# Optimization experiments

Hardware: AMD Instinct MI355X
Metric: run time of the kernel (lower is better)

## Reference

```python
import jax, jax.numpy as jnp
import numpy as np

B, T, D, H = 8, 2048, 1024, 128


def setup_inputs() -> dict:
    key = jax.random.key(0)
    k1, k2, k3, k4 = jax.random.split(key, 4)
    x = jax.random.normal(k1, (B, T, D), dtype=jnp.float32)
    # nn.Linear(D, H, bias=False): y = x @ W.T with W [H, D]; we store W as [D, H]
    Wq = jax.random.normal(k2, (D, H), dtype=jnp.float32) * (1.0 / np.sqrt(D))
    Wk = jax.random.normal(k3, (D, H), dtype=jnp.float32) * (1.0 / np.sqrt(D))
    Wv = jax.random.normal(k4, (D, H), dtype=jnp.float32) * (1.0 / np.sqrt(D))
    return {"x": x, "Wq": Wq, "Wk": Wk, "Wv": Wv}


def reference(x, Wq, Wk, Wv):
    # q, k, v projections (bias-free)
    q = jnp.einsum("btd,dh->bth", x, Wq)
    k = jnp.einsum("btd,dh->bth", x, Wk)
    v = jnp.einsum("btd,dh->bth", x, Wv)
    scale = 1.0 / jnp.sqrt(jnp.asarray(q.shape[-1], dtype=q.dtype))
    # full T x T score matrix, as in the original module
    scores = jnp.einsum("bqh,bkh->bqk", q, k) * scale
    T_ = x.shape[1]
    causal = jnp.tril(jnp.ones((T_, T_), dtype=bool))
    scores = jnp.where(causal[None, :, :], scores, -jnp.inf)
    weights = jax.nn.softmax(scores, axis=-1)
    # dropout is identity in eval mode (deterministic reference)
    return jnp.einsum("bqk,bkh->bqh", weights, v)
```

## Files before the change

kernel.cpp:

```cpp
#include <hip/hip_runtime.h>

typedef float  f32x4  __attribute__((ext_vector_type(4)));
typedef __bf16 bf16x8 __attribute__((ext_vector_type(8)));
typedef unsigned short u16;
typedef unsigned int   u32;
typedef u32 u32x4 __attribute__((ext_vector_type(4)));
typedef u16 u16x4 __attribute__((ext_vector_type(4)));
typedef u16 u16x8 __attribute__((ext_vector_type(8)));
typedef float f32x4v __attribute__((ext_vector_type(4)));

#define B_ 8
#define T_ 2048
#define D_ 1024
#define H_ 128
#define M_ (B_ * T_)

__device__ __forceinline__ u16 f2b(float f) {
  u32 u = __builtin_bit_cast(u32, f);
  u32 r = u + 0x7fffu + ((u >> 16) & 1u);
  return (u16)(r >> 16);
}

__device__ __forceinline__ void gl2lds16(const void* g, void* l) {
  __builtin_amdgcn_global_load_lds(
      (const __attribute__((address_space(1))) void*)g,
      (__attribute__((address_space(3))) void*)l, 16, 0, 0);
}

__global__ __launch_bounds__(256) void wt_kernel(const float* __restrict__ Wq,
                                                 const float* __restrict__ Wk,
                                                 const float* __restrict__ Wv,
                                                 u16* __restrict__ ws) {
  __shared__ u16 Ld[128 * 136];
  const float* W = (blockIdx.y == 0) ? Wq : (blockIdx.y == 1) ? Wk : Wv;
  u16* Wt = ws + (size_t)blockIdx.y * (D_ * H_);
  const int d0 = blockIdx.x * 128;
  const int t = threadIdx.x;
  for (int i = 0; i < 16; ++i) {
    int idx = i * 256 + t;
    int d = idx >> 5, h4 = (idx & 31) * 4;
    f32x4v wv = *(const f32x4v*)(W + (size_t)(d0 + d) * H_ + h4);
    u16x4 bv;
    bv[0] = f2b(wv[0]); bv[1] = f2b(wv[1]); bv[2] = f2b(wv[2]); bv[3] = f2b(wv[3]);
    *(u16x4*)(&Ld[d * 136 + h4]) = bv;
  }
  __syncthreads();
  for (int i = 0; i < 8; ++i) {
    int idx = i * 256 + t;
    int h = idx >> 4, d8 = (idx & 15) * 8;
    u16x8 ov;
    for (int j = 0; j < 8; ++j) ov[j] = Ld[(d8 + j) * 136 + h];
    *(u16x8*)(Wt + (size_t)h * D_ + d0 + d8) = ov;
  }
}

__global__ __launch_bounds__(512, 4) void qkv_gemm(const float* __restrict__ x,
                                                   const u16* __restrict__ Wt_all,
                                                   u16* __restrict__ Qb,
                                                   u16* __restrict__ Kb,
                                                   u16* __restrict__ Vt) {
  __shared__ __attribute__((aligned(16))) u16 As[2][64 * 40];
  __shared__ __attribute__((aligned(16))) u16 Bs[2][192 * 40];
  const int m0 = (int)(blockIdx.x >> 1) * 64;
  const int n0 = (int)(blockIdx.x & 1) * 192;
  const int t = threadIdx.x;
  const int lane = t & 63;
  const int w = t >> 6;
  const int wm = (w & 1) * 32, wn = (w >> 1) * 48;
  const int li = lane & 15, q4 = lane >> 4;

  const int arow = t >> 3, ac4 = (t & 7) * 4;

  f32x4 acc[2][3];
  for (int i = 0; i < 2; ++i)
    for (int j = 0; j < 3; ++j) acc[i][j] = (f32x4){0.f, 0.f, 0.f, 0.f};

  f32x4v areg[2];
  u16x4 breg[2][3];

  auto load_tiles = [&](int kt, int s) {
    const int k0 = kt * 32;
    areg[s] = *(const f32x4v*)(x + (size_t)(m0 + arow) * D_ + k0 + ac4);
    for (int i2 = 0; i2 < 3; ++i2) {
      int idx = i2 * 512 + t;
      int row = idx >> 3, c4 = (idx & 7) * 4;
      breg[s][i2] = *(const u16x4*)(Wt_all + (size_t)(n0 + row) * D_ + k0 + c4);
    }
  };

  load_tiles(0, 0);
  load_tiles(1, 1);
  for (int kt = 0; kt < 32; ++kt) {
    const int s = kt & 1;
    {
      u16x4 av;
      av[0] = f2b(areg[s][0]); av[1] = f2b(areg[s][1]);
      av[2] = f2b(areg[s][2]); av[3] = f2b(areg[s][3]);
      *(u16x4*)(&As[s][arow * 40 + ac4]) = av;
    }
    for (int i2 = 0; i2 < 3; ++i2) {
      int idx = i2 * 512 + t;
      int row = idx >> 3, c4 = (idx & 7) * 4;
      *(u16x4*)(&Bs[s][row * 40 + c4]) = breg[s][i2];
    }
    __syncthreads();
    if (kt + 2 < 32) load_tiles(kt + 2, s);

    bf16x8 af[2];
    for (int i = 0; i < 2; ++i)
      af[i] = *(const bf16x8*)(&As[s][(wm + i * 16 + li) * 40 + q4 * 8]);
    for (int j = 0; j < 3; ++j) {
      bf16x8 bfr = *(const bf16x8*)(&Bs[s][(wn + j * 16 + li) * 40 + q4 * 8]);
      for (int i = 0; i < 2; ++i)
        acc[i][j] = __builtin_amdgcn_mfma_f32_16x16x32_bf16(af[i], bfr, acc[i][j], 0, 0, 0);
    }
  }

  const float qs = 0.12751740696864213f;
  const int bb = m0 >> 11;
  const int tl0 = (m0 & (T_ - 1)) + wm + q4 * 4;
  for (int j = 0; j < 3; ++j) {
    int n = n0 + wn + j * 16 + li;
    int p = n >> 7, col = n & 127;
    if (p == 2) {
      for (int i = 0; i < 2; ++i) {
        u16x4 pv;
        for (int r = 0; r < 4; ++r) pv[r] = f2b(acc[i][j][r]);
        *(u16x4*)(Vt + (size_t)bb * (H_ * T_) + (size_t)col * T_ + tl0 + i * 16) = pv;
      }
    } else {
      u16* dst = (p == 0) ? Qb : Kb;
      float s = (p == 0) ? qs : 1.0f;
      for (int i = 0; i < 2; ++i)
        for (int r = 0; r < 4; ++r) {
          int mg = m0 + wm + i * 16 + q4 * 4 + r;
          dst[(size_t)mg * H_ + col] = f2b(acc[i][j][r] * s);
        }
    }
  }
}

#define NSLOT_PER_B 36

__device__ __forceinline__ int slot_base(int qt) {
  return (qt < 8) ? 2 * (qt - 4) : (qt < 12) ? 8 + 3 * (qt - 8) : 20 + 4 * (qt - 12);
}

__global__ __launch_bounds__(512, 2) void flash_split(const u16* __restrict__ Qb,
                                                      const u16* __restrict__ Kb,
                                                      const u16* __restrict__ Vt,
                                                      float* __restrict__ Opart,
                                                      float* __restrict__ Ls,
                                                      float* __restrict__ out) {
  __shared__ __attribute__((aligned(16))) u16 Ks[64 * 128];
  __shared__ __attribute__((aligned(16))) u16 Vs[128 * 64];
  __shared__ __attribute__((aligned(16))) u16 Ps[128 * 72];

  int xb = blockIdx.x, qt = 15, split = 0;
  for (int q = 15; q >= 0; --q) {
    int ns = (2 * q + 9) >> 3;
    if (xb < ns) { qt = q; split = xb; break; }
    xb -= ns;
  }
  const int b = blockIdx.y;
  const int nkv = 2 * qt + 2;
  const int nsplit = (2 * qt + 9) >> 3;
  const int kv0t = split * 8;
  const int kv1t = (kv0t + 8 < nkv) ? kv0t + 8 : nkv;
  const int q0 = qt * 128;

  const int t = threadIdx.x;
  const int lane = t & 63;
  const int w = t >> 6;
  const int li = lane & 15, q4 = lane >> 4;

  bf16x8 qf[4];
  const int qrow = b * T_ + q0 + w * 16 + li;
  for (int kk = 0; kk < 4; ++kk)
    qf[kk] = *(const bf16x8*)(Qb + (size_t)qrow * H_ + kk * 32 + q4 * 8);

  f32x4 oacc[8];
  for (int i = 0; i < 8; ++i) oacc[i] = (f32x4){0.f, 0.f, 0.f, 0.f};
  float rs[4] = {0.f, 0.f, 0.f, 0.f};

  for (int jt = kv0t; jt < kv1t; ++jt) {
    const int j0 = jt * 64;
    __syncthreads();
    for (int i = 0; i < 2; ++i) {
      int seg = i * 8 + w;
      {
        int r = seg * 4 + (lane >> 4);
        int c = (lane & 15) ^ (r & 7);
        gl2lds16(Kb + (size_t)(b * T_ + j0 + r) * H_ + c * 8, &Ks[seg << 9]);
      }
      {
        int r = seg * 8 + (lane >> 3);
        int c = (lane & 7) ^ (r & 7);
        gl2lds16(Vt + (size_t)b * (H_ * T_) + (size_t)r * T_ + j0 + c * 8,
                 &Vs[seg << 9]);
      }
    }
    __syncthreads();

    f32x4 sacc[4];
    for (int jn = 0; jn < 4; ++jn) sacc[jn] = (f32x4){0.f, 0.f, 0.f, 0.f};
    for (int jn = 0; jn < 4; ++jn) {
      int row = jn * 16 + li;
      for (int kk = 0; kk < 4; ++kk) {
        int phys = ((kk << 2) | q4) ^ (row & 7);
        bf16x8 kf = *(const bf16x8*)(&Ks[row * 128 + phys * 8]);
        sacc[jn] = __builtin_amdgcn_mfma_f32_16x16x32_bf16(qf[kk], kf, sacc[jn], 0, 0, 0);
      }
    }

    if (jt >= 2 * qt) {
      for (int jn = 0; jn < 4; ++jn) {
        int jg = j0 + jn * 16 + li;
        for (int r = 0; r < 4; ++r) {
          int qg = q0 + w * 16 + q4 * 4 + r;
          if (jg > qg) sacc[jn][r] = -1e30f;
        }
      }
    }

    for (int jn = 0; jn < 4; ++jn)
      for (int r = 0; r < 4; ++r) {
        float p = exp2f(sacc[jn][r]);
        rs[r] += p;
        Ps[(w * 16 + q4 * 4 + r) * 72 + jn * 16 + li] = f2b(p);
      }

    for (int ks = 0; ks < 2; ++ks) {
      bf16x8 pa = *(const bf16x8*)(&Ps[(w * 16 + li) * 72 + ks * 32 + q4 * 8]);
      for (int hn = 0; hn < 8; ++hn) {
        int row = hn * 16 + li;
        int phys = ((ks << 2) | q4) ^ (row & 7);
        bf16x8 vf = *(const bf16x8*)(&Vs[row * 64 + phys * 8]);
        oacc[hn] = __builtin_amdgcn_mfma_f32_16x16x32_bf16(pa, vf, oacc[hn], 0, 0, 0);
      }
    }
  }

  float lr[4];
  for (int r = 0; r < 4; ++r) {
    float s = rs[r];
    for (int off = 1; off < 16; off <<= 1) s += __shfl_xor(s, off, 16);
    lr[r] = s;
  }

  if (nsplit == 1) {
    for (int hn = 0; hn < 8; ++hn)
      for (int r = 0; r < 4; ++r) {
        int qg = b * T_ + q0 + w * 16 + q4 * 4 + r;
        out[(size_t)qg * H_ + hn * 16 + li] = oacc[hn][r] / lr[r];
      }
  } else {
    const int slot = b * NSLOT_PER_B + slot_base(qt) + split;
    float* Od = Opart + (size_t)slot * (128 * 128);
    for (int hn = 0; hn < 8; ++hn)
      for (int r = 0; r < 4; ++r) {
        int qq = w * 16 + q4 * 4 + r;
        Od[qq * 128 + hn * 16 + li] = oacc[hn][r];
      }
    if (li == 0)
      for (int r = 0; r < 4; ++r)
        Ls[slot * 128 + w * 16 + q4 * 4 + r] = lr[r];
  }
}

__global__ __launch_bounds__(512) void flash_merge(const float* __restrict__ Opart,
                                                   const float* __restrict__ Ls,
                                                   float* __restrict__ out) {
  __shared__ float inv_l[128];
  const int qt = 4 + blockIdx.x;
  const int b = blockIdx.y;
  const int nsplit = (2 * qt + 9) >> 3;
  const int slot0 = b * NSLOT_PER_B + slot_base(qt);
  const int t = threadIdx.x;

  if (t < 128) {
    float L = 0.f;
    for (int s = 0; s < nsplit; ++s) L += Ls[(slot0 + s) * 128 + t];
    inv_l[t] = 1.0f / L;
  }
  __syncthreads();

  float* dst = out + ((size_t)b * T_ + (size_t)qt * 128) * H_;
  for (int i = 0; i < 8; ++i) {
    int e4 = i * 512 + t;
    int q = e4 >> 5;
    f32x4 acc = (f32x4){0.f, 0.f, 0.f, 0.f};
    for (int s = 0; s < nsplit; ++s) {
      f32x4 v = *(const f32x4*)(Opart + (size_t)(slot0 + s) * (128 * 128) + e4 * 4);
      acc[0] += v[0]; acc[1] += v[1]; acc[2] += v[2]; acc[3] += v[3];
    }
    float inv = inv_l[q];
    acc[0] *= inv; acc[1] *= inv; acc[2] *= inv; acc[3] *= inv;
    *(f32x4*)(dst + e4 * 4) = acc;
  }
}

extern "C" void kernel_launch(void* const* d_in, const int* in_sizes, int n_in,
                              void* d_out, int out_size, void* d_ws, size_t ws_size,
                              hipStream_t stream) {
  const float* x  = (const float*)d_in[0];
  const float* Wq = (const float*)d_in[1];
  const float* Wk = (const float*)d_in[2];
  const float* Wv = (const float*)d_in[3];
  float* out = (float*)d_out;

  u16* ws = (u16*)d_ws;
  u16* WtAll = ws;
  u16* Qb = ws + 3 * (size_t)(D_ * H_);
  u16* Kb = Qb + (size_t)M_ * H_;
  u16* Vt = Kb + (size_t)M_ * H_;
  float* Opart = (float*)(Vt + (size_t)M_ * H_);
  float* Ls = Opart + (size_t)8 * NSLOT_PER_B * 128 * 128;

  wt_kernel<<<dim3(8, 3), 256, 0, stream>>>(Wq, Wk, Wv, WtAll);
  qkv_gemm<<<dim3(512), 512, 0, stream>>>(x, WtAll, Qb, Kb, Vt);
  flash_split<<<dim3(40, 8), 512, 0, stream>>>(Qb, Kb, Vt, Opart, Ls, out);
  flash_merge<<<dim3(12, 8), 512, 0, stream>>>(Opart, Ls, out);
}
```

Baseline: 173.8 us.

## Double-buffer K/V in flash kernel, stage GEMM B tiles directly to LDS

The flash attention kernel now double-buffers the K and V tiles in shared memory. The next tile's direct global-to-LDS loads are issued right after the barrier, so they overlap the current tile's MFMA work. The QKV GEMM loads the weight tile straight into a swizzled, unpadded LDS layout, which removes the register round trip. It also cuts the A prefetch to one tile ahead. The weight transpose kernel uses smaller 32-row blocks to launch more workgroups. Doubling K/V LDS raises shared memory use per block and may lower occupancy. The shallower A prefetch can expose global load latency in the GEMM.

```diff
diff --git a/kernel.cpp b/kernel.cpp
--- a/kernel.cpp
+++ b/kernel.cpp
@@ -31,12 +31,12 @@
                                                  const float* __restrict__ Wk,
                                                  const float* __restrict__ Wv,
                                                  u16* __restrict__ ws) {
-  __shared__ u16 Ld[128 * 136];
+  __shared__ u16 Ld[32 * 136];
   const float* W = (blockIdx.y == 0) ? Wq : (blockIdx.y == 1) ? Wk : Wv;
   u16* Wt = ws + (size_t)blockIdx.y * (D_ * H_);
-  const int d0 = blockIdx.x * 128;
+  const int d0 = blockIdx.x * 32;
   const int t = threadIdx.x;
-  for (int i = 0; i < 16; ++i) {
+  for (int i = 0; i < 4; ++i) {
     int idx = i * 256 + t;
     int d = idx >> 5, h4 = (idx & 31) * 4;
     f32x4v wv = *(const f32x4v*)(W + (size_t)(d0 + d) * H_ + h4);
@@ -45,9 +45,9 @@
     *(u16x4*)(&Ld[d * 136 + h4]) = bv;
   }
   __syncthreads();
-  for (int i = 0; i < 8; ++i) {
+  for (int i = 0; i < 2; ++i) {
     int idx = i * 256 + t;
-    int h = idx >> 4, d8 = (idx & 15) * 8;
+    int h = idx >> 2, d8 = (idx & 3) * 8;
     u16x8 ov;
     for (int j = 0; j < 8; ++j) ov[j] = Ld[(d8 + j) * 136 + h];
     *(u16x8*)(Wt + (size_t)h * D_ + d0 + d8) = ov;
@@ -60,7 +60,7 @@
                                                    u16* __restrict__ Kb,
                                                    u16* __restrict__ Vt) {
   __shared__ __attribute__((aligned(16))) u16 As[2][64 * 40];
-  __shared__ __attribute__((aligned(16))) u16 Bs[2][192 * 40];
+  __shared__ __attribute__((aligned(16))) u16 Bs[2][192 * 32];
   const int m0 = (int)(blockIdx.x >> 1) * 64;
   const int n0 = (int)(blockIdx.x & 1) * 192;
   const int t = threadIdx.x;
@@ -68,49 +68,46 @@
   const int w = t >> 6;
   const int wm = (w & 1) * 32, wn = (w >> 1) * 48;
   const int li = lane & 15, q4 = lane >> 4;
-
   const int arow = t >> 3, ac4 = (t & 7) * 4;
+  const int br = lane >> 2, bu = lane & 3;
+  const int bul = bu ^ ((br >> 1) & 3);
 
   f32x4 acc[2][3];
   for (int i = 0; i < 2; ++i)
     for (int j = 0; j < 3; ++j) acc[i][j] = (f32x4){0.f, 0.f, 0.f, 0.f};
 
-  f32x4v areg[2];
-  u16x4 breg[2][3];
-
-  auto load_tiles = [&](int kt, int s) {
-    const int k0 = kt * 32;
-    areg[s] = *(const f32x4v*)(x + (size_t)(m0 + arow) * D_ + k0 + ac4);
-    for (int i2 = 0; i2 < 3; ++i2) {
-      int idx = i2 * 512 + t;
-      int row = idx >> 3, c4 = (idx & 7) * 4;
-      breg[s][i2] = *(const u16x4*)(Wt_all + (size_t)(n0 + row) * D_ + k0 + c4);
-    }
+  f32x4v areg;
+  auto load_a = [&](int kt) {
+    areg = *(const f32x4v*)(x + (size_t)(m0 + arow) * D_ + kt * 32 + ac4);
   };
-
-  load_tiles(0, 0);
-  load_tiles(1, 1);
+  auto stage_b = [&](int kt, int sb) {
+    for (int ii = 0; ii < 2; ++ii) {
+      int seg = ii * 8 + w;
+      if (seg < 12)
+        gl2lds16(Wt_all + (size_t)(n0 + seg * 16 + br) * D_ + kt * 32 + bul * 8,
+                 &Bs[sb][seg * 512]);
+    }
+  };
+
+  load_a(0);
+  stage_b(0, 0);
   for (int kt = 0; kt < 32; ++kt) {
     const int s = kt & 1;
     {
       u16x4 av;
-      av[0] = f2b(areg[s][0]); av[1] = f2b(areg[s][1]);
-      av[2] = f2b(areg[s][2]); av[3] = f2b(areg[s][3]);
+      av[0] = f2b(areg[0]); av[1] = f2b(areg[1]);
+      av[2] = f2b(areg[2]); av[3] = f2b(areg[3]);
       *(u16x4*)(&As[s][arow * 40 + ac4]) = av;
     }
-    for (int i2 = 0; i2 < 3; ++i2) {
-      int idx = i2 * 512 + t;
-      int row = idx >> 3, c4 = (idx & 7) * 4;
-      *(u16x4*)(&Bs[s][row * 40 + c4]) = breg[s][i2];
-    }
     __syncthreads();
-    if (kt + 2 < 32) load_tiles(kt + 2, s);
+    if (kt + 1 < 32) { load_a(kt + 1); stage_b(kt + 1, s ^ 1); }
 
     bf16x8 af[2];
     for (int i = 0; i < 2; ++i)
       af[i] = *(const bf16x8*)(&As[s][(wm + i * 16 + li) * 40 + q4 * 8]);
     for (int j = 0; j < 3; ++j) {
-      bf16x8 bfr = *(const bf16x8*)(&Bs[s][(wn + j * 16 + li) * 40 + q4 * 8]);
+      int R = wn + j * 16 + li;
+      bf16x8 bfr = *(const bf16x8*)(&Bs[s][R * 32 + (q4 ^ ((li >> 1) & 3)) * 8]);
       for (int i = 0; i < 2; ++i)
         acc[i][j] = __builtin_amdgcn_mfma_f32_16x16x32_bf16(af[i], bfr, acc[i][j], 0, 0, 0);
     }
@@ -130,11 +127,11 @@
       }
     } else {
       u16* dst = (p == 0) ? Qb : Kb;
-      float s = (p == 0) ? qs : 1.0f;
+      float sc = (p == 0) ? qs : 1.0f;
       for (int i = 0; i < 2; ++i)
         for (int r = 0; r < 4; ++r) {
           int mg = m0 + wm + i * 16 + q4 * 4 + r;
-          dst[(size_t)mg * H_ + col] = f2b(acc[i][j][r] * s);
+          dst[(size_t)mg * H_ + col] = f2b(acc[i][j][r] * sc);
         }
     }
   }
@@ -152,8 +149,8 @@
                                                       float* __restrict__ Opart,
                                                       float* __restrict__ Ls,
                                                       float* __restrict__ out) {
-  __shared__ __attribute__((aligned(16))) u16 Ks[64 * 128];
-  __shared__ __attribute__((aligned(16))) u16 Vs[128 * 64];
+  __shared__ __attribute__((aligned(16))) u16 Ks[2][64 * 128];
+  __shared__ __attribute__((aligned(16))) u16 Vs[2][128 * 64];
   __shared__ __attribute__((aligned(16))) u16 Ps[128 * 72];
 
   int xb = blockIdx.x, qt = 15, split = 0;
@@ -183,24 +180,30 @@
   for (int i = 0; i < 8; ++i) oacc[i] = (f32x4){0.f, 0.f, 0.f, 0.f};
   float rs[4] = {0.f, 0.f, 0.f, 0.f};
 
-  for (int jt = kv0t; jt < kv1t; ++jt) {
+  auto stage = [&](int jt, int sb) {
     const int j0 = jt * 64;
-    __syncthreads();
     for (int i = 0; i < 2; ++i) {
       int seg = i * 8 + w;
       {
         int r = seg * 4 + (lane >> 4);
         int c = (lane & 15) ^ (r & 7);
-        gl2lds16(Kb + (size_t)(b * T_ + j0 + r) * H_ + c * 8, &Ks[seg << 9]);
+        gl2lds16(Kb + (size_t)(b * T_ + j0 + r) * H_ + c * 8, &Ks[sb][seg << 9]);
       }
       {
         int r = seg * 8 + (lane >> 3);
         int c = (lane & 7) ^ (r & 7);
         gl2lds16(Vt + (size_t)b * (H_ * T_) + (size_t)r * T_ + j0 + c * 8,
-                 &Vs[seg << 9]);
-      }
-    }
+                 &Vs[sb][seg << 9]);
+      }
+    }
+  };
+
+  stage(kv0t, 0);
+  for (int jt = kv0t; jt < kv1t; ++jt) {
+    const int buf = (jt - kv0t) & 1;
+    const int j0 = jt * 64;
     __syncthreads();
+    if (jt + 1 < kv1t) stage(jt + 1, buf ^ 1);
 
     f32x4 sacc[4];
     for (int jn = 0; jn < 4; ++jn) sacc[jn] = (f32x4){0.f, 0.f, 0.f, 0.f};
@@ -208,7 +211,7 @@
       int row = jn * 16 + li;
       for (int kk = 0; kk < 4; ++kk) {
         int phys = ((kk << 2) | q4) ^ (row & 7);
-        bf16x8 kf = *(const bf16x8*)(&Ks[row * 128 + phys * 8]);
+        bf16x8 kf = *(const bf16x8*)(&Ks[buf][row * 128 + phys * 8]);
         sacc[jn] = __builtin_amdgcn_mfma_f32_16x16x32_bf16(qf[kk], kf, sacc[jn], 0, 0, 0);
       }
     }
@@ -235,7 +238,7 @@
       for (int hn = 0; hn < 8; ++hn) {
         int row = hn * 16 + li;
         int phys = ((ks << 2) | q4) ^ (row & 7);
-        bf16x8 vf = *(const bf16x8*)(&Vs[row * 64 + phys * 8]);
+        bf16x8 vf = *(const bf16x8*)(&Vs[buf][row * 64 + phys * 8]);
         oacc[hn] = __builtin_amdgcn_mfma_f32_16x16x32_bf16(pa, vf, oacc[hn], 0, 0, 0);
       }
     }
@@ -317,7 +320,7 @@
   float* Opart = (float*)(Vt + (size_t)M_ * H_);
   float* Ls = Opart + (size_t)8 * NSLOT_PER_B * 128 * 128;
 
-  wt_kernel<<<dim3(8, 3), 256, 0, stream>>>(Wq, Wk, Wv, WtAll);
+  wt_kernel<<<dim3(32, 3), 256, 0, stream>>>(Wq, Wk, Wv, WtAll);
   qkv_gemm<<<dim3(512), 512, 0, stream>>>(x, WtAll, Qb, Kb, Vt);
   flash_split<<<dim3(40, 8), 512, 0, stream>>>(Qb, Kb, Vt, Opart, Ls, out);
   flash_merge<<<dim3(12, 8), 512, 0, stream>>>(Opart, Ls, out);
```

After: 179.2 us. 1.03x slower.
